# Optimization experiments

Hardware: AMD Instinct MI355X
Metric: run time of the kernel (lower is better)

Reference implementation:

```python
import jax, jax.numpy as jnp
import numpy as np

DEPTH, HEADS, DIM_HEAD = 6, 12, 64
DIM, MLP, FEAT = 768, 3072, 1000
B, N = 32, 196
EPS = 1e-5


def layernorm(x, g, b):
    m = jnp.mean(x, axis=-1, keepdims=True)
    v = jnp.var(x, axis=-1, keepdims=True)
    return (x - m) * jax.lax.rsqrt(v + EPS) * g + b


def setup_inputs() -> dict:
    key = jax.random.key(0)
    ks = jax.random.split(key, 8)
    s = 0.02
    return {
        "x": jax.random.normal(ks[0], (B, N, DIM), jnp.float32),
        "cls_token": jax.random.normal(ks[1], (1, 1, DIM), jnp.float32),
        "ln1_g": jnp.ones((DEPTH, DIM), jnp.float32),
        "ln1_b": jnp.zeros((DEPTH, DIM), jnp.float32),
        "w_qkv": jax.random.normal(ks[2], (DEPTH, DIM, 3 * HEADS * DIM_HEAD), jnp.float32) * s,
        "reattn_w": jax.random.normal(ks[3], (DEPTH, HEADS, HEADS), jnp.float32),
        "reattn_g": jnp.ones((DEPTH, HEADS), jnp.float32),
        "reattn_b": jnp.zeros((DEPTH, HEADS), jnp.float32),
        "w_out": jax.random.normal(ks[4], (DEPTH, HEADS * DIM_HEAD, DIM), jnp.float32) * s,
        "b_out": jnp.zeros((DEPTH, DIM), jnp.float32),
        "ln2_g": jnp.ones((DEPTH, DIM), jnp.float32),
        "ln2_b": jnp.zeros((DEPTH, DIM), jnp.float32),
        "w1": jax.random.normal(ks[5], (DEPTH, DIM, MLP), jnp.float32) * s,
        "b1": jnp.zeros((DEPTH, MLP), jnp.float32),
        "w2": jax.random.normal(ks[6], (DEPTH, MLP, DIM), jnp.float32) * s,
        "b2": jnp.zeros((DEPTH, DIM), jnp.float32),
        "lnf_g": jnp.ones((DIM,), jnp.float32),
        "lnf_b": jnp.zeros((DIM,), jnp.float32),
        "w_head": jax.random.normal(ks[7], (DIM, FEAT), jnp.float32) * s,
        "b_head": jnp.zeros((FEAT,), jnp.float32),
    }


def _forward(x, cls_token, ln1_g, ln1_b, w_qkv, reattn_w, reattn_g, reattn_b,
             w_out, b_out, ln2_g, ln2_b, w1, b1, w2, b2, lnf_g, lnf_b, w_head, b_head):
    b = x.shape[0]
    cls = jnp.broadcast_to(cls_token, (b, 1, DIM))
    x = jnp.concatenate([cls, x], axis=1)  # (B, N+1, DIM)
    n = x.shape[1]
    scale = DIM_HEAD ** -0.5
    for l in range(DEPTH):
        h = layernorm(x, ln1_g[l], ln1_b[l])
        qkv = h @ w_qkv[l]                       # (B, n, 3*H*Dh)
        qkv = qkv.reshape(b, n, 3, HEADS, DIM_HEAD)
        q, k, v = (qkv[:, :, i].transpose(0, 2, 1, 3) for i in range(3))  # b h n d
        dots = jnp.einsum('bhid,bhjd->bhij', q, k) * scale
        attn = jax.nn.softmax(dots, axis=-1)
        attn = jnp.einsum('bhij,hg->bgij', attn, reattn_w[l])
        # per-head LayerNorm: normalize over head axis (axis=1)
        m = jnp.mean(attn, axis=1, keepdims=True)
        var = jnp.var(attn, axis=1, keepdims=True)
        attn = (attn - m) * jax.lax.rsqrt(var + EPS)
        attn = attn * reattn_g[l][None, :, None, None] + reattn_b[l][None, :, None, None]
        out = jnp.einsum('bhij,bhjd->bhid', attn, v)
        out = out.transpose(0, 2, 1, 3).reshape(b, n, HEADS * DIM_HEAD)
        x = x + out @ w_out[l] + b_out[l]
        h = layernorm(x, ln2_g[l], ln2_b[l])
        h = jax.nn.gelu(h @ w1[l] + b1[l], approximate=False)
        x = x + h @ w2[l] + b2[l]
    pooled = x[:, 0]  # cls pool
    return layernorm(pooled, lnf_g, lnf_b) @ w_head + b_head


def reference(x, cls_token, ln1_g, ln1_b, w_qkv, reattn_w, reattn_g, reattn_b,
              w_out, b_out, ln2_g, ln2_b, w1, b1, w2, b2, lnf_g, lnf_b, w_head, b_head):
    return _forward(x, cls_token, ln1_g, ln1_b, w_qkv, reattn_w, reattn_g, reattn_b,
                    w_out, b_out, ln2_g, ln2_b, w1, b1, w2, b2, lnf_g, lnf_b, w_head, b_head)
```

## Files before the change

### kernel.cpp

```cpp
#include <hip/hip_runtime.h>
#include <cstdint>

typedef __bf16 bf16_t;
typedef __bf16 bf16x8 __attribute__((ext_vector_type(8)));
typedef float  f32x4  __attribute__((ext_vector_type(4)));
typedef unsigned int u32;

#define DEPTH 6
#define HEADS 12
#define DH    64
#define DIM   768
#define MLPD  3072
#define FEAT  1000
#define BATCH 32
#define SEQ   197
#define NP    224
#define TOK   (BATCH*SEQ)

__device__ __forceinline__ f32x4 zero4() {
    f32x4 z; z[0] = 0.f; z[1] = 0.f; z[2] = 0.f; z[3] = 0.f; return z;
}

__device__ __forceinline__ f32x4 mfma16(bf16x8 a, bf16x8 b, f32x4 c) {
    return __builtin_amdgcn_mfma_f32_16x16x32_bf16(a, b, c, 0, 0, 0);
}

typedef const __attribute__((address_space(1))) u32* gas_ptr;
typedef __attribute__((address_space(3))) u32*       las_ptr;
__device__ __forceinline__ void gload16(const bf16_t* g, bf16_t* l) {
    __builtin_amdgcn_global_load_lds((gas_ptr)g, (las_ptr)l, 16, 0, 0);
}

__global__ __launch_bounds__(256) void concat_k(const float* __restrict__ x,
                                                const float* __restrict__ cls,
                                                float* __restrict__ xbuf) {
    int idx = blockIdx.x * 256 + threadIdx.x;
    int col = idx % DIM;
    int row = idx / DIM;
    int b = row / SEQ, p = row % SEQ;
    xbuf[idx] = (p == 0) ? cls[col] : x[(b * 196 + p - 1) * DIM + col];
}

__global__ __launch_bounds__(256) void tcvt_k(const float* __restrict__ W,
                                              bf16_t* __restrict__ Wt,
                                              int K, int N) {
    __shared__ float t[32][33];
    int n0 = blockIdx.x * 32, k0 = blockIdx.y * 32;
    int c = threadIdx.x & 31, r = threadIdx.x >> 5;
#pragma unroll
    for (int i = 0; i < 4; i++) {
        int k = k0 + r + i * 8, n = n0 + c;
        t[r + i * 8][c] = (n < N) ? W[k * N + n] : 0.f;
    }
    __syncthreads();
#pragma unroll
    for (int i = 0; i < 4; i++) {
        int n = n0 + r + i * 8, k = k0 + c;
        if (n < N) Wt[n * K + k] = (bf16_t)t[c][r + i * 8];
    }
}

__global__ __launch_bounds__(256) void ln_k(const float* __restrict__ x, long row_stride,
                                            const float* __restrict__ g,
                                            const float* __restrict__ b,
                                            bf16_t* __restrict__ out) {
    int row = blockIdx.x;
    const float* xr = x + (long)row * row_stride;
    int t = threadIdx.x;
    float v0 = xr[t], v1 = xr[t + 256], v2 = xr[t + 512];
    float s  = v0 + v1 + v2;
    float sq = v0 * v0 + v1 * v1 + v2 * v2;
#pragma unroll
    for (int o = 1; o < 64; o <<= 1) { s += __shfl_xor(s, o); sq += __shfl_xor(sq, o); }
    __shared__ float ss[4], sqs[4];
    int w = t >> 6;
    if ((t & 63) == 0) { ss[w] = s; sqs[w] = sq; }
    __syncthreads();
    s  = ss[0] + ss[1] + ss[2] + ss[3];
    sq = sqs[0] + sqs[1] + sqs[2] + sqs[3];
    float m  = s * (1.f / 768.f);
    float rs = rsqrtf(sq * (1.f / 768.f) - m * m + 1e-5f);
    bf16_t* orow = out + (long)row * DIM;
    orow[t]       = (bf16_t)((v0 - m) * rs * g[t]       + b[t]);
    orow[t + 256] = (bf16_t)((v1 - m) * rs * g[t + 256] + b[t + 256]);
    orow[t + 512] = (bf16_t)((v2 - m) * rs * g[t + 512] + b[t + 512]);
}

template <int MODE>
__global__ __launch_bounds__(256) void gemm_k(const bf16_t* __restrict__ A,
                                              const bf16_t* __restrict__ Bt,
                                              const float* __restrict__ bias,
                                              float* __restrict__ Cf,
                                              bf16_t* __restrict__ Cb,
                                              int M, int N, int K) {
    __shared__ bf16_t sA[2][128][32];
    __shared__ bf16_t sB[2][128][32];
    int tid = threadIdx.x;
    int bm = blockIdx.x * 128, bn = blockIdx.y * 128;
    int wave = tid >> 6, lane = tid & 63;
    int wm = (wave >> 1) * 64, wn = (wave & 1) * 64;
    int la = lane & 15, lb = lane >> 4;

    int rowA[2], rowB[2], colE[2];
#pragma unroll
    for (int q = 0; q < 2; q++) {
        int li = (wave * 2 + q) * 64 + lane;
        int row = li >> 2;
        colE[q] = (li & 3) * 8;
        int ar = bm + row; if (ar > M - 1) ar = M - 1;
        int br = bn + row; if (br > N - 1) br = N - 1;
        rowA[q] = ar; rowB[q] = br;
    }

    f32x4 acc[4][4];
#pragma unroll
    for (int m = 0; m < 4; m++)
#pragma unroll
        for (int n = 0; n < 4; n++) acc[m][n] = zero4();

    int nt = K >> 5;

#pragma unroll
    for (int q = 0; q < 2; q++) {
        gload16(A  + (long)rowA[q] * K + colE[q], &sA[0][0][0] + (wave * 2 + q) * 512);
        gload16(Bt + (long)rowB[q] * K + colE[q], &sB[0][0][0] + (wave * 2 + q) * 512);
    }
    __syncthreads();

    for (int t = 0; t < nt; t++) {
        int cur = t & 1;
        if (t + 1 < nt) {
            int k0 = (t + 1) << 5;
#pragma unroll
            for (int q = 0; q < 2; q++) {
                gload16(A  + (long)rowA[q] * K + k0 + colE[q], &sA[cur ^ 1][0][0] + (wave * 2 + q) * 512);
                gload16(Bt + (long)rowB[q] * K + k0 + colE[q], &sB[cur ^ 1][0][0] + (wave * 2 + q) * 512);
            }
        }
        bf16x8 af[4], bfr[4];
#pragma unroll
        for (int m = 0; m < 4; m++) af[m]  = *(const bf16x8*)&sA[cur][wm + m * 16 + la][lb * 8];
#pragma unroll
        for (int n = 0; n < 4; n++) bfr[n] = *(const bf16x8*)&sB[cur][wn + n * 16 + la][lb * 8];
#pragma unroll
        for (int m = 0; m < 4; m++)
#pragma unroll
            for (int n = 0; n < 4; n++)
                acc[m][n] = mfma16(af[m], bfr[n], acc[m][n]);
        __syncthreads();
    }

#pragma unroll
    for (int m = 0; m < 4; m++) {
#pragma unroll
        for (int n = 0; n < 4; n++) {
            int ib = bm + wm + m * 16 + lb * 4;
            int jb = bn + wn + n * 16 + la;
            if (jb >= N) continue;
            float bv = (MODE == 0) ? 0.f : bias[jb];
#pragma unroll
            for (int r = 0; r < 4; r++) {
                int i = ib + r;
                if (i >= M) continue;
                float v = acc[m][n][r];
                if (MODE == 0) {
                    Cb[(long)i * N + jb] = (bf16_t)v;
                } else if (MODE == 1) {
                    Cf[(long)i * N + jb] += v + bv;
                } else if (MODE == 2) {
                    float u = v + bv;
                    Cb[(long)i * N + jb] = (bf16_t)(0.5f * u * (1.f + erff(u * 0.70710678118f)));
                } else {
                    Cf[(long)i * N + jb] = v + bv;
                }
            }
        }
    }
}

__global__ __launch_bounds__(256) void qk_k(const bf16_t* __restrict__ qkv,
                                            float* __restrict__ dots) {
    int bh = blockIdx.z;
    int b = bh / HEADS, h = bh % HEADS;
    int i0 = blockIdx.x * 64, j0 = blockIdx.y * 64;
    __shared__ bf16_t sQ[64][32], sK[64][32];
    int tid = threadIdx.x, wave = tid >> 6, lane = tid & 63;
    int wm = (wave >> 1) * 32, wn = (wave & 1) * 32;
    int la = lane & 15, lb = lane >> 4;
    f32x4 acc[2][2];
#pragma unroll
    for (int m = 0; m < 2; m++)
#pragma unroll
        for (int n = 0; n < 2; n++) acc[m][n] = zero4();

    int row = tid >> 2, col = (tid & 3) * 8;
    int qi = i0 + row; if (qi > SEQ - 1) qi = SEQ - 1;
    int kj = j0 + row; if (kj > SEQ - 1) kj = SEQ - 1;
    const bf16_t* qsrc = qkv + (((b * SEQ + qi) * 3 + 0) * HEADS + h) * DH + col;
    const bf16_t* ksrc = qkv + (((b * SEQ + kj) * 3 + 1) * HEADS + h) * DH + col;

#pragma unroll
    for (int d0 = 0; d0 < 64; d0 += 32) {
        *(bf16x8*)&sQ[row][col] = *(const bf16x8*)(qsrc + d0);
        *(bf16x8*)&sK[row][col] = *(const bf16x8*)(ksrc + d0);
        __syncthreads();
        bf16x8 af[2], bfr[2];
#pragma unroll
        for (int m = 0; m < 2; m++) af[m]  = *(const bf16x8*)&sQ[wm + m * 16 + la][lb * 8];
#pragma unroll
        for (int n = 0; n < 2; n++) bfr[n] = *(const bf16x8*)&sK[wn + n * 16 + la][lb * 8];
#pragma unroll
        for (int m = 0; m < 2; m++)
#pragma unroll
            for (int n = 0; n < 2; n++)
                acc[m][n] = mfma16(af[m], bfr[n], acc[m][n]);
        __syncthreads();
    }
#pragma unroll
    for (int m = 0; m < 2; m++)
#pragma unroll
        for (int n = 0; n < 2; n++)
#pragma unroll
            for (int r = 0; r < 4; r++) {
                int i = i0 + wm + m * 16 + lb * 4 + r;
                int j = j0 + wn + n * 16 + la;
                if (i < SEQ && j < SEQ)
                    dots[((long)bh * SEQ + i) * NP + j] = acc[m][n][r] * 0.125f;
            }
}

__global__ __launch_bounds__(256) void smre_k(const float* __restrict__ dots,
                                              const float* __restrict__ W,
                                              const float* __restrict__ gg,
                                              const float* __restrict__ bb,
                                              bf16_t* __restrict__ attn2) {
    __shared__ float sm[HEADS][NP];
    __shared__ float sW[HEADS * HEADS];
    __shared__ float sg[HEADS], sb[HEADS];
    int tid = threadIdx.x;
    if (tid < HEADS * HEADS) sW[tid] = W[tid];
    if (tid < HEADS) { sg[tid] = gg[tid]; sb[tid] = bb[tid]; }
    int bi = blockIdx.x;
    int b = bi / SEQ, i = bi % SEQ;
    int wave = tid >> 6, lane = tid & 63;

    for (int h = wave; h < HEADS; h += 4) {
        const float* p = dots + ((long)(b * HEADS + h) * SEQ + i) * NP;
        float v[4], e[4];
#pragma unroll
        for (int q = 0; q < 4; q++) { int j = lane + 64 * q; v[q] = (j < SEQ) ? p[j] : -3.0e38f; }
        float mx = fmaxf(fmaxf(v[0], v[1]), fmaxf(v[2], v[3]));
#pragma unroll
        for (int o = 1; o < 64; o <<= 1) mx = fmaxf(mx, __shfl_xor(mx, o));
        float s = 0.f;
#pragma unroll
        for (int q = 0; q < 4; q++) {
            int j = lane + 64 * q;
            e[q] = (j < SEQ) ? __expf(v[q] - mx) : 0.f;
            s += e[q];
        }
#pragma unroll
        for (int o = 1; o < 64; o <<= 1) s += __shfl_xor(s, o);
        float inv = 1.f / s;
#pragma unroll
        for (int q = 0; q < 4; q++) { int j = lane + 64 * q; if (j < NP) sm[h][j] = e[q] * inv; }
    }
    __syncthreads();

    int j = tid;
    if (j >= NP) return;
    bool valid = j < SEQ;
    float vals[HEADS];
#pragma unroll
    for (int h = 0; h < HEADS; h++) vals[h] = valid ? sm[h][j] : 0.f;
    float mix[HEADS];
    float s = 0.f, sq = 0.f;
#pragma unroll
    for (int g = 0; g < HEADS; g++) {
        float a = 0.f;
#pragma unroll
        for (int h = 0; h < HEADS; h++) a += vals[h] * sW[h * HEADS + g];
        mix[g] = a; s += a; sq += a * a;
    }
    float m  = s * (1.f / 12.f);
    float rs = rsqrtf(sq * (1.f / 12.f) - m * m + 1e-5f);
    long base = ((long)(b * HEADS) * SEQ + i) * NP + j;
    const long hs = (long)SEQ * NP;
#pragma unroll
    for (int g = 0; g < HEADS; g++) {
        float o = valid ? ((mix[g] - m) * rs * sg[g] + sb[g]) : 0.f;
        attn2[base + g * hs] = (bf16_t)o;
    }
}

__global__ __launch_bounds__(256) void pv_k(const bf16_t* __restrict__ attn2,
                                            const bf16_t* __restrict__ qkv,
                                            bf16_t* __restrict__ aout) {
    int bh = blockIdx.y;
    int b = bh / HEADS, h = bh % HEADS;
    int i0 = blockIdx.x * 64;
    __shared__ bf16_t sP[64][32];
    __shared__ bf16_t sVt[64][32];
    int tid = threadIdx.x, wave = tid >> 6, lane = tid & 63;
    int wm = (wave >> 1) * 32, wn = (wave & 1) * 32;
    int la = lane & 15, lb = lane >> 4;
    f32x4 acc[2][2];
#pragma unroll
    for (int m = 0; m < 2; m++)
#pragma unroll
        for (int n = 0; n < 2; n++) acc[m][n] = zero4();

    int prow = tid >> 2, pcol = (tid & 3) * 8;
    int pi = i0 + prow; if (pi > SEQ - 1) pi = SEQ - 1;
    const bf16_t* psrc = attn2 + ((long)bh * SEQ + pi) * NP + pcol;
    int jl = tid >> 3, dblk = (tid & 7) * 8;
    int jlx = jl ^ ((tid & 3) << 3);

    for (int j0 = 0; j0 < NP; j0 += 32) {
        *(bf16x8*)&sP[prow][pcol] = *(const bf16x8*)(psrc + j0);
        int jg = j0 + jl;
        bf16x8 vv;
#pragma unroll
        for (int e = 0; e < 8; e++) vv[e] = (bf16_t)0.f;
        if (jg < SEQ)
            vv = *(const bf16x8*)(qkv + (((b * SEQ + jg) * 3 + 2) * HEADS + h) * DH + dblk);
#pragma unroll
        for (int e = 0; e < 8; e++) sVt[dblk + e][jlx] = vv[e];
        __syncthreads();
        bf16x8 af[2], bfr[2];
#pragma unroll
        for (int m = 0; m < 2; m++) af[m] = *(const bf16x8*)&sP[wm + m * 16 + la][lb * 8];
#pragma unroll
        for (int n = 0; n < 2; n++) {
            int rowd = wn + n * 16 + la;
            int colj = (lb * 8) ^ (((rowd >> 3) & 3) << 3);
            bfr[n] = *(const bf16x8*)&sVt[rowd][colj];
        }
#pragma unroll
        for (int m = 0; m < 2; m++)
#pragma unroll
            for (int n = 0; n < 2; n++)
                acc[m][n] = mfma16(af[m], bfr[n], acc[m][n]);
        __syncthreads();
    }
#pragma unroll
    for (int m = 0; m < 2; m++)
#pragma unroll
        for (int n = 0; n < 2; n++)
#pragma unroll
            for (int r = 0; r < 4; r++) {
                int i = i0 + wm + m * 16 + lb * 4 + r;
                int d = wn + n * 16 + la;
                if (i < SEQ)
                    aout[((long)b * SEQ + i) * DIM + h * DH + d] = (bf16_t)acc[m][n][r];
            }
}

extern "C" void kernel_launch(void* const* d_in, const int* in_sizes, int n_in,
                              void* d_out, int out_size, void* d_ws, size_t ws_size,
                              hipStream_t stream) {
    const float* x        = (const float*)d_in[0];
    const float* cls      = (const float*)d_in[1];
    const float* ln1_g    = (const float*)d_in[2];
    const float* ln1_b    = (const float*)d_in[3];
    const float* w_qkv    = (const float*)d_in[4];
    const float* reattn_w = (const float*)d_in[5];
    const float* reattn_g = (const float*)d_in[6];
    const float* reattn_b = (const float*)d_in[7];
    const float* w_out    = (const float*)d_in[8];
    const float* b_out    = (const float*)d_in[9];
    const float* ln2_g    = (const float*)d_in[10];
    const float* ln2_b    = (const float*)d_in[11];
    const float* w1       = (const float*)d_in[12];
    const float* b1       = (const float*)d_in[13];
    const float* w2       = (const float*)d_in[14];
    const float* b2       = (const float*)d_in[15];
    const float* lnf_g    = (const float*)d_in[16];
    const float* lnf_b    = (const float*)d_in[17];
    const float* w_head   = (const float*)d_in[18];
    const float* b_head   = (const float*)d_in[19];
    float* out = (float*)d_out;

    char* p = (char*)d_ws;
    auto alloc = [&](size_t bytes) -> char* {
        char* r = p;
        p += (bytes + 255) & ~(size_t)255;
        return r;
    };
    bf16_t* wt      = (bf16_t*)alloc(2ULL * MLPD * DIM);
    bf16_t* wt_head = (bf16_t*)alloc(2ULL * FEAT * DIM);
    float*  xbuf    = (float*)alloc(4ULL * TOK * DIM);
    bf16_t* h_ln    = (bf16_t*)alloc(2ULL * TOK * DIM);
    bf16_t* qkv     = (bf16_t*)alloc(2ULL * TOK * 3 * DIM);
    float*  dots    = (float*)alloc(4ULL * BATCH * HEADS * SEQ * NP);
    bf16_t* h_mid   = (bf16_t*)dots;
    bf16_t* attn2   = (bf16_t*)alloc(2ULL * BATCH * HEADS * SEQ * NP);
    bf16_t* aout    = (bf16_t*)alloc(2ULL * TOK * DIM);

    dim3 B256(256);
    concat_k<<<(TOK * DIM) / 256, B256, 0, stream>>>(x, cls, xbuf);
    tcvt_k<<<dim3((FEAT + 31) / 32, DIM / 32), B256, 0, stream>>>(w_head, wt_head, DIM, FEAT);

    for (int l = 0; l < DEPTH; l++) {
        ln_k<<<TOK, B256, 0, stream>>>(xbuf, DIM, ln1_g + l * DIM, ln1_b + l * DIM, h_ln);
        tcvt_k<<<dim3(2304 / 32, DIM / 32), B256, 0, stream>>>(w_qkv + (long)l * DIM * 2304, wt, DIM, 2304);
        gemm_k<0><<<dim3(50, 18), B256, 0, stream>>>(h_ln, wt, nullptr, nullptr, qkv, TOK, 2304, DIM);
        qk_k<<<dim3(4, 4, BATCH * HEADS), B256, 0, stream>>>(qkv, dots);
        smre_k<<<TOK, B256, 0, stream>>>(
            dots, reattn_w + l * HEADS * HEADS, reattn_g + l * HEADS, reattn_b + l * HEADS, attn2);
        pv_k<<<dim3(4, BATCH * HEADS), B256, 0, stream>>>(attn2, qkv, aout);
        tcvt_k<<<dim3(DIM / 32, DIM / 32), B256, 0, stream>>>(w_out + (long)l * DIM * DIM, wt, DIM, DIM);
        gemm_k<1><<<dim3(50, 6), B256, 0, stream>>>(aout, wt, b_out + l * DIM, xbuf, nullptr, TOK, DIM, DIM);
        ln_k<<<TOK, B256, 0, stream>>>(xbuf, DIM, ln2_g + l * DIM, ln2_b + l * DIM, h_ln);
        tcvt_k<<<dim3(MLPD / 32, DIM / 32), B256, 0, stream>>>(w1 + (long)l * DIM * MLPD, wt, DIM, MLPD);
        gemm_k<2><<<dim3(50, 24), B256, 0, stream>>>(h_ln, wt, b1 + l * MLPD, nullptr, h_mid, TOK, MLPD, DIM);
        tcvt_k<<<dim3(DIM / 32, MLPD / 32), B256, 0, stream>>>(w2 + (long)l * MLPD * DIM, wt, MLPD, DIM);
        gemm_k<1><<<dim3(50, 6), B256, 0, stream>>>(h_mid, wt, b2 + l * DIM, xbuf, nullptr, TOK, DIM, MLPD);
    }

    ln_k<<<BATCH, B256, 0, stream>>>(xbuf, (long)SEQ * DIM, lnf_g, lnf_b, h_ln);
    gemm_k<3><<<dim3(1, 8), B256, 0, stream>>>(h_ln, wt_head, b_head, out, nullptr, BATCH, FEAT, DIM);
}
```

Measured before the change: 2.143 ms.

## Replace layer GEMMs with 256x256 eight-wave MFMA kernel using swizzled LDS

Adds gemm8_k, a 512-thread kernel that computes 256x256 tiles with BK=64. It uses XOR-swizzled LDS layouts, loads directly from global memory into LDS two stages ahead, and splits each k-step into four MFMA quadrants with barriers and setprio interleaving. The QKV, out-projection, MLP1 and MLP2 GEMMs now use it, while the head GEMM stays on a simplified 128x128 kernel. The goals are more data reuse per tile, fewer LDS bank conflicts and better overlap of loads with MFMA work. The cost is heavy register use at one block per CU and coarse tiles: with 6304 rows there are 25 row tiles, which gives only 75 blocks for the N=768 GEMMs, so the GPU may be underfilled.

```diff
diff --git a/kernel.cpp b/kernel.cpp
--- a/kernel.cpp
+++ b/kernel.cpp
@@ -29,6 +29,11 @@
 typedef __attribute__((address_space(3))) u32*       las_ptr;
 __device__ __forceinline__ void gload16(const bf16_t* g, bf16_t* l) {
     __builtin_amdgcn_global_load_lds((gas_ptr)g, (las_ptr)l, 16, 0, 0);
+}
+
+__device__ __forceinline__ void bar() {
+    __builtin_amdgcn_s_barrier();
+    asm volatile("" ::: "memory");
 }
 
 __global__ __launch_bounds__(256) void concat_k(const float* __restrict__ x,
@@ -86,12 +91,170 @@
     orow[t + 512] = (bf16_t)((v2 - m) * rs * g[t + 512] + b[t + 512]);
 }
 
+#define MFMAQ(mh, nh)                                                        \
+    _Pragma("unroll")                                                        \
+    for (int mf = 0; mf < 4; mf++) {                                         \
+        _Pragma("unroll")                                                    \
+        for (int nf = 0; nf < 2; nf++) {                                     \
+            f32x4 c = acc[(mh) * 2 + (nh)][mf * 2 + nf];                     \
+            c = mfma16(aR[mf][0], bR[nh][nf][0], c);                         \
+            c = mfma16(aR[mf][1], bR[nh][nf][1], c);                         \
+            acc[(mh) * 2 + (nh)][mf * 2 + nf] = c;                           \
+        }                                                                    \
+    }
+
 template <int MODE>
-__global__ __launch_bounds__(256) void gemm_k(const bf16_t* __restrict__ A,
+__global__ __launch_bounds__(512, 1) void gemm8_k(const bf16_t* __restrict__ A,
+                                                  const bf16_t* __restrict__ Bt,
+                                                  const float* __restrict__ bias,
+                                                  float* __restrict__ Cf,
+                                                  bf16_t* __restrict__ Cb,
+                                                  int M, int N, int K, int gn) {
+    __shared__ bf16_t sA[2][256 * 64];
+    __shared__ bf16_t sB[2][256 * 64];
+    int tid = threadIdx.x;
+    int bm = (blockIdx.x / gn) * 256, bn = (blockIdx.x % gn) * 256;
+    int wave = tid >> 6, lane = tid & 63;
+    int wm = (wave >> 2) * 128, wn = (wave & 3) * 64;
+    int la = lane & 15, lb = lane >> 4;
+
+    int srow = tid >> 3;
+    int scol = ((tid & 7) ^ (srow & 7)) * 8;
+    int rA[4], rB[4];
+#pragma unroll
+    for (int i = 0; i < 4; i++) {
+        int r = bm + i * 64 + srow; rA[i] = (r < M) ? r : M - 1;
+        rB[i] = bn + i * 64 + srow;
+    }
+    int woff = wave * 512;
+
+    f32x4 acc[4][8];
+#pragma unroll
+    for (int q = 0; q < 4; q++)
+#pragma unroll
+        for (int f = 0; f < 8; f++) acc[q][f] = zero4();
+    bf16x8 aR[4][2], bR[2][2][2];
+
+    const int NT = K >> 6;
+
+    auto stA = [&](int buf, int kt) {
+        long k0 = (long)kt << 6;
+#pragma unroll
+        for (int i = 0; i < 4; i++)
+            gload16(A + (long)rA[i] * K + k0 + scol, &sA[buf][0] + i * 4096 + woff);
+    };
+    auto stB = [&](int buf, int kt) {
+        long k0 = (long)kt << 6;
+#pragma unroll
+        for (int i = 0; i < 4; i++)
+            gload16(Bt + (long)rB[i] * K + k0 + scol, &sB[buf][0] + i * 4096 + woff);
+    };
+
+    stB(0, 0); stA(0, 0); stB(1, 1); stA(1, 1);
+    asm volatile("s_waitcnt vmcnt(8)" ::: "memory");
+    bar();
+
+    for (int t = 0; t < NT; t++) {
+        const bf16_t* cA = &sA[t & 1][0];
+        const bf16_t* cB = &sB[t & 1][0];
+        bool st = (t + 2) < NT;
+
+#pragma unroll
+        for (int mf = 0; mf < 4; mf++)
+#pragma unroll
+            for (int ks = 0; ks < 2; ks++) {
+                int r = wm + mf * 16 + la, gl = ks * 4 + lb;
+                aR[mf][ks] = *(const bf16x8*)(cA + r * 64 + ((gl ^ (r & 7)) << 3));
+            }
+#pragma unroll
+        for (int nf = 0; nf < 2; nf++)
+#pragma unroll
+            for (int ks = 0; ks < 2; ks++) {
+                int r = wn + nf * 16 + la, gl = ks * 4 + lb;
+                bR[0][nf][ks] = *(const bf16x8*)(cB + r * 64 + ((gl ^ (r & 7)) << 3));
+            }
+        bar();
+        asm volatile("s_waitcnt lgkmcnt(0)" ::: "memory");
+        __builtin_amdgcn_sched_barrier(0);
+        __builtin_amdgcn_s_setprio(1);
+        MFMAQ(0, 0)
+        __builtin_amdgcn_s_setprio(0);
+        bar();
+
+#pragma unroll
+        for (int nf = 0; nf < 2; nf++)
+#pragma unroll
+            for (int ks = 0; ks < 2; ks++) {
+                int r = wn + 32 + nf * 16 + la, gl = ks * 4 + lb;
+                bR[1][nf][ks] = *(const bf16x8*)(cB + r * 64 + ((gl ^ (r & 7)) << 3));
+            }
+        bar();
+        asm volatile("s_waitcnt lgkmcnt(0)" ::: "memory");
+        __builtin_amdgcn_sched_barrier(0);
+        __builtin_amdgcn_s_setprio(1);
+        MFMAQ(0, 1)
+        __builtin_amdgcn_s_setprio(0);
+        bar();
+
+#pragma unroll
+        for (int mf = 0; mf < 4; mf++)
+#pragma unroll
+            for (int ks = 0; ks < 2; ks++) {
+                int r = wm + 64 + mf * 16 + la, gl = ks * 4 + lb;
+                aR[mf][ks] = *(const bf16x8*)(cA + r * 64 + ((gl ^ (r & 7)) << 3));
+            }
+        if (st) stB(t & 1, t + 2);
+        bar();
+        asm volatile("s_waitcnt lgkmcnt(0)" ::: "memory");
+        __builtin_amdgcn_sched_barrier(0);
+        __builtin_amdgcn_s_setprio(1);
+        MFMAQ(1, 1)
+        __builtin_amdgcn_s_setprio(0);
+        bar();
+
+        if (st) stA(t & 1, t + 2);
+        __builtin_amdgcn_s_setprio(1);
+        MFMAQ(1, 0)
+        __builtin_amdgcn_s_setprio(0);
+        if (t < NT - 1) {
+            if (st) asm volatile("s_waitcnt vmcnt(8)" ::: "memory");
+            else    asm volatile("s_waitcnt vmcnt(0)" ::: "memory");
+            bar();
+        }
+    }
+
+#pragma unroll
+    for (int mh = 0; mh < 2; mh++)
+#pragma unroll
+        for (int nh = 0; nh < 2; nh++)
+#pragma unroll
+            for (int mf = 0; mf < 4; mf++)
+#pragma unroll
+                for (int nf = 0; nf < 2; nf++) {
+                    int ib = bm + wm + mh * 64 + mf * 16 + lb * 4;
+                    int jb = bn + wn + nh * 32 + nf * 16 + la;
+                    float bv = (MODE == 0) ? 0.f : bias[jb];
+                    f32x4 v = acc[mh * 2 + nh][mf * 2 + nf];
+#pragma unroll
+                    for (int rr = 0; rr < 4; rr++) {
+                        int i = ib + rr;
+                        if (i >= M) continue;
+                        if (MODE == 0) {
+                            Cb[(long)i * N + jb] = (bf16_t)v[rr];
+                        } else if (MODE == 1) {
+                            Cf[(long)i * N + jb] += v[rr] + bv;
+                        } else {
+                            float u = v[rr] + bv;
+                            Cb[(long)i * N + jb] = (bf16_t)(0.5f * u * (1.f + erff(u * 0.70710678118f)));
+                        }
+                    }
+                }
+}
+
+__global__ __launch_bounds__(256) void gemm_h(const bf16_t* __restrict__ A,
                                               const bf16_t* __restrict__ Bt,
                                               const float* __restrict__ bias,
                                               float* __restrict__ Cf,
-                                              bf16_t* __restrict__ Cb,
                                               int M, int N, int K) {
     __shared__ bf16_t sA[2][128][32];
     __shared__ bf16_t sB[2][128][32];
@@ -100,7 +263,6 @@
     int wave = tid >> 6, lane = tid & 63;
     int wm = (wave >> 1) * 64, wn = (wave & 1) * 64;
     int la = lane & 15, lb = lane >> 4;
-
     int rowA[2], rowB[2], colE[2];
 #pragma unroll
     for (int q = 0; q < 2; q++) {
@@ -111,22 +273,18 @@
         int br = bn + row; if (br > N - 1) br = N - 1;
         rowA[q] = ar; rowB[q] = br;
     }
-
     f32x4 acc[4][4];
 #pragma unroll
     for (int m = 0; m < 4; m++)
 #pragma unroll
         for (int n = 0; n < 4; n++) acc[m][n] = zero4();
-
     int nt = K >> 5;
-
 #pragma unroll
     for (int q = 0; q < 2; q++) {
         gload16(A  + (long)rowA[q] * K + colE[q], &sA[0][0][0] + (wave * 2 + q) * 512);
         gload16(Bt + (long)rowB[q] * K + colE[q], &sB[0][0][0] + (wave * 2 + q) * 512);
     }
     __syncthreads();
-
     for (int t = 0; t < nt; t++) {
         int cur = t & 1;
         if (t + 1 < nt) {
@@ -149,7 +307,6 @@
                 acc[m][n] = mfma16(af[m], bfr[n], acc[m][n]);
         __syncthreads();
     }
-
 #pragma unroll
     for (int m = 0; m < 4; m++) {
 #pragma unroll
@@ -157,22 +314,12 @@
             int ib = bm + wm + m * 16 + lb * 4;
             int jb = bn + wn + n * 16 + la;
             if (jb >= N) continue;
-            float bv = (MODE == 0) ? 0.f : bias[jb];
+            float bv = bias[jb];
 #pragma unroll
             for (int r = 0; r < 4; r++) {
                 int i = ib + r;
                 if (i >= M) continue;
-                float v = acc[m][n][r];
-                if (MODE == 0) {
-                    Cb[(long)i * N + jb] = (bf16_t)v;
-                } else if (MODE == 1) {
-                    Cf[(long)i * N + jb] += v + bv;
-                } else if (MODE == 2) {
-                    float u = v + bv;
-                    Cb[(long)i * N + jb] = (bf16_t)(0.5f * u * (1.f + erff(u * 0.70710678118f)));
-                } else {
-                    Cf[(long)i * N + jb] = v + bv;
-                }
+                Cf[(long)i * N + jb] = acc[m][n][r] + bv;
             }
         }
     }
@@ -397,27 +544,28 @@
     bf16_t* attn2   = (bf16_t*)alloc(2ULL * BATCH * HEADS * SEQ * NP);
     bf16_t* aout    = (bf16_t*)alloc(2ULL * TOK * DIM);
 
-    dim3 B256(256);
+    dim3 B256(256), B512(512);
+    const int GM = (TOK + 255) / 256;
     concat_k<<<(TOK * DIM) / 256, B256, 0, stream>>>(x, cls, xbuf);
     tcvt_k<<<dim3((FEAT + 31) / 32, DIM / 32), B256, 0, stream>>>(w_head, wt_head, DIM, FEAT);
 
     for (int l = 0; l < DEPTH; l++) {
         ln_k<<<TOK, B256, 0, stream>>>(xbuf, DIM, ln1_g + l * DIM, ln1_b + l * DIM, h_ln);
         tcvt_k<<<dim3(2304 / 32, DIM / 32), B256, 0, stream>>>(w_qkv + (long)l * DIM * 2304, wt, DIM, 2304);
-        gemm_k<0><<<dim3(50, 18), B256, 0, stream>>>(h_ln, wt, nullptr, nullptr, qkv, TOK, 2304, DIM);
+        gemm8_k<0><<<GM * 9, B512, 0, stream>>>(h_ln, wt, nullptr, nullptr, qkv, TOK, 2304, DIM, 9);
         qk_k<<<dim3(4, 4, BATCH * HEADS), B256, 0, stream>>>(qkv, dots);
         smre_k<<<TOK, B256, 0, stream>>>(
             dots, reattn_w + l * HEADS * HEADS, reattn_g + l * HEADS, reattn_b + l * HEADS, attn2);
         pv_k<<<dim3(4, BATCH * HEADS), B256, 0, stream>>>(attn2, qkv, aout);
         tcvt_k<<<dim3(DIM / 32, DIM / 32), B256, 0, stream>>>(w_out + (long)l * DIM * DIM, wt, DIM, DIM);
-        gemm_k<1><<<dim3(50, 6), B256, 0, stream>>>(aout, wt, b_out + l * DIM, xbuf, nullptr, TOK, DIM, DIM);
+        gemm8_k<1><<<GM * 3, B512, 0, stream>>>(aout, wt, b_out + l * DIM, xbuf, nullptr, TOK, DIM, DIM, 3);
         ln_k<<<TOK, B256, 0, stream>>>(xbuf, DIM, ln2_g + l * DIM, ln2_b + l * DIM, h_ln);
         tcvt_k<<<dim3(MLPD / 32, DIM / 32), B256, 0, stream>>>(w1 + (long)l * DIM * MLPD, wt, DIM, MLPD);
-        gemm_k<2><<<dim3(50, 24), B256, 0, stream>>>(h_ln, wt, b1 + l * MLPD, nullptr, h_mid, TOK, MLPD, DIM);
+        gemm8_k<2><<<GM * 12, B512, 0, stream>>>(h_ln, wt, b1 + l * MLPD, nullptr, h_mid, TOK, MLPD, DIM, 12);
         tcvt_k<<<dim3(DIM / 32, MLPD / 32), B256, 0, stream>>>(w2 + (long)l * MLPD * DIM, wt, MLPD, DIM);
-        gemm_k<1><<<dim3(50, 6), B256, 0, stream>>>(h_mid, wt, b2 + l * DIM, xbuf, nullptr, TOK, DIM, MLPD);
+        gemm8_k<1><<<GM * 3, B512, 0, stream>>>(h_mid, wt, b2 + l * DIM, xbuf, nullptr, TOK, DIM, MLPD, 3);
     }
 
     ln_k<<<BATCH, B256, 0, stream>>>(xbuf, (long)SEQ * DIM, lnf_g, lnf_b, h_ln);
-    gemm_k<3><<<dim3(1, 8), B256, 0, stream>>>(h_ln, wt_head, b_head, out, nullptr, BATCH, FEAT, DIM);
-}
+    gemm_h<<<dim3(1, 8), B256, 0, stream>>>(h_ln, wt_head, b_head, out, BATCH, FEAT, DIM);
+}
```

New measurement: 2.804 ms. +30.8%, slower.

## Fuse softmax/re-attention with PV matmul and split-K the MLP down projection

Applied to the files above, without the earlier changes.

The separate softmax+re-attention kernel and the PV kernel become one kernel that processes 8 query rows across all 12 heads per block. It keeps the mixed attention probabilities in shared memory and multiplies them with V directly, so the bf16 attn2 intermediate no longer goes through global memory. The MLP second GEMM is split into two K halves across a grid z dimension, writing fp32 partials that a new reduction kernel adds into the residual along with the bias. A dedicated head GEMM kernel replaces the old mode-3 path. The costs are a large shared-memory footprint per block, 8-row MFMA tiles that leave half of each 16-row fragment unused, and extra fp32 partial traffic for the split-K.

```diff
diff --git a/kernel.cpp b/kernel.cpp
--- a/kernel.cpp
+++ b/kernel.cpp
@@ -16,6 +16,7 @@
 #define SEQ   197
 #define NP    224
 #define TOK   (BATCH*SEQ)
+#define ITILES 25
 
 __device__ __forceinline__ f32x4 zero4() {
     f32x4 z; z[0] = 0.f; z[1] = 0.f; z[2] = 0.f; z[3] = 0.f; return z;
@@ -92,11 +93,12 @@
                                               const float* __restrict__ bias,
                                               float* __restrict__ Cf,
                                               bf16_t* __restrict__ Cb,
-                                              int M, int N, int K) {
+                                              int M, int N, int Kstride, int Klen) {
     __shared__ bf16_t sA[2][128][32];
     __shared__ bf16_t sB[2][128][32];
     int tid = threadIdx.x;
     int bm = blockIdx.x * 128, bn = blockIdx.y * 128;
+    long koff = (long)blockIdx.z * Klen;
     int wave = tid >> 6, lane = tid & 63;
     int wm = (wave >> 1) * 64, wn = (wave & 1) * 64;
     int la = lane & 15, lb = lane >> 4;
@@ -118,23 +120,21 @@
 #pragma unroll
         for (int n = 0; n < 4; n++) acc[m][n] = zero4();
 
-    int nt = K >> 5;
-
+    int nt = Klen >> 5;
 #pragma unroll
     for (int q = 0; q < 2; q++) {
-        gload16(A  + (long)rowA[q] * K + colE[q], &sA[0][0][0] + (wave * 2 + q) * 512);
-        gload16(Bt + (long)rowB[q] * K + colE[q], &sB[0][0][0] + (wave * 2 + q) * 512);
+        gload16(A  + (long)rowA[q] * Kstride + koff + colE[q], &sA[0][0][0] + (wave * 2 + q) * 512);
+        gload16(Bt + (long)rowB[q] * Kstride + koff + colE[q], &sB[0][0][0] + (wave * 2 + q) * 512);
     }
     __syncthreads();
-
     for (int t = 0; t < nt; t++) {
         int cur = t & 1;
         if (t + 1 < nt) {
-            int k0 = (t + 1) << 5;
+            long k0 = koff + ((t + 1) << 5);
 #pragma unroll
             for (int q = 0; q < 2; q++) {
-                gload16(A  + (long)rowA[q] * K + k0 + colE[q], &sA[cur ^ 1][0][0] + (wave * 2 + q) * 512);
-                gload16(Bt + (long)rowB[q] * K + k0 + colE[q], &sB[cur ^ 1][0][0] + (wave * 2 + q) * 512);
+                gload16(A  + (long)rowA[q] * Kstride + k0 + colE[q], &sA[cur ^ 1][0][0] + (wave * 2 + q) * 512);
+                gload16(Bt + (long)rowB[q] * Kstride + k0 + colE[q], &sB[cur ^ 1][0][0] + (wave * 2 + q) * 512);
             }
         }
         bf16x8 af[4], bfr[4];
@@ -150,6 +150,7 @@
         __syncthreads();
     }
 
+    long kout = (long)blockIdx.z * M * (long)N;
 #pragma unroll
     for (int m = 0; m < 4; m++) {
 #pragma unroll
@@ -157,7 +158,7 @@
             int ib = bm + wm + m * 16 + lb * 4;
             int jb = bn + wn + n * 16 + la;
             if (jb >= N) continue;
-            float bv = (MODE == 0) ? 0.f : bias[jb];
+            float bv = (MODE == 1 || MODE == 2) ? bias[jb] : 0.f;
 #pragma unroll
             for (int r = 0; r < 4; r++) {
                 int i = ib + r;
@@ -171,8 +172,92 @@
                     float u = v + bv;
                     Cb[(long)i * N + jb] = (bf16_t)(0.5f * u * (1.f + erff(u * 0.70710678118f)));
                 } else {
-                    Cf[(long)i * N + jb] = v + bv;
+                    Cf[kout + (long)i * N + jb] = v;
                 }
+            }
+        }
+    }
+}
+
+__global__ __launch_bounds__(256) void redk_k(float* __restrict__ xbuf,
+                                              const float* __restrict__ part,
+                                              const float* __restrict__ bias) {
+    const long total = (long)TOK * DIM;
+    for (long idx = blockIdx.x * 256 + threadIdx.x; idx < total; idx += (long)gridDim.x * 256) {
+        int col = (int)(idx % DIM);
+        xbuf[idx] += part[idx] + part[idx + total] + bias[col];
+    }
+}
+
+__global__ __launch_bounds__(256) void gemm_h(const bf16_t* __restrict__ A,
+                                              const bf16_t* __restrict__ Bt,
+                                              const float* __restrict__ bias,
+                                              float* __restrict__ Cf,
+                                              int M, int N, int K) {
+    __shared__ bf16_t sA[2][128][32];
+    __shared__ bf16_t sB[2][128][32];
+    int tid = threadIdx.x;
+    int bm = blockIdx.x * 128, bn = blockIdx.y * 128;
+    int wave = tid >> 6, lane = tid & 63;
+    int wm = (wave >> 1) * 64, wn = (wave & 1) * 64;
+    int la = lane & 15, lb = lane >> 4;
+    int rowA[2], rowB[2], colE[2];
+#pragma unroll
+    for (int q = 0; q < 2; q++) {
+        int li = (wave * 2 + q) * 64 + lane;
+        int row = li >> 2;
+        colE[q] = (li & 3) * 8;
+        int ar = bm + row; if (ar > M - 1) ar = M - 1;
+        int br = bn + row; if (br > N - 1) br = N - 1;
+        rowA[q] = ar; rowB[q] = br;
+    }
+    f32x4 acc[4][4];
+#pragma unroll
+    for (int m = 0; m < 4; m++)
+#pragma unroll
+        for (int n = 0; n < 4; n++) acc[m][n] = zero4();
+    int nt = K >> 5;
+#pragma unroll
+    for (int q = 0; q < 2; q++) {
+        gload16(A  + (long)rowA[q] * K + colE[q], &sA[0][0][0] + (wave * 2 + q) * 512);
+        gload16(Bt + (long)rowB[q] * K + colE[q], &sB[0][0][0] + (wave * 2 + q) * 512);
+    }
+    __syncthreads();
+    for (int t = 0; t < nt; t++) {
+        int cur = t & 1;
+        if (t + 1 < nt) {
+            int k0 = (t + 1) << 5;
+#pragma unroll
+            for (int q = 0; q < 2; q++) {
+                gload16(A  + (long)rowA[q] * K + k0 + colE[q], &sA[cur ^ 1][0][0] + (wave * 2 + q) * 512);
+                gload16(Bt + (long)rowB[q] * K + k0 + colE[q], &sB[cur ^ 1][0][0] + (wave * 2 + q) * 512);
+            }
+        }
+        bf16x8 af[4], bfr[4];
+#pragma unroll
+        for (int m = 0; m < 4; m++) af[m]  = *(const bf16x8*)&sA[cur][wm + m * 16 + la][lb * 8];
+#pragma unroll
+        for (int n = 0; n < 4; n++) bfr[n] = *(const bf16x8*)&sB[cur][wn + n * 16 + la][lb * 8];
+#pragma unroll
+        for (int m = 0; m < 4; m++)
+#pragma unroll
+            for (int n = 0; n < 4; n++)
+                acc[m][n] = mfma16(af[m], bfr[n], acc[m][n]);
+        __syncthreads();
+    }
+#pragma unroll
+    for (int m = 0; m < 4; m++) {
+#pragma unroll
+        for (int n = 0; n < 4; n++) {
+            int ib = bm + wm + m * 16 + lb * 4;
+            int jb = bn + wn + n * 16 + la;
+            if (jb >= N) continue;
+            float bv = bias[jb];
+#pragma unroll
+            for (int r = 0; r < 4; r++) {
+                int i = ib + r;
+                if (i >= M) continue;
+                Cf[(long)i * N + jb] = acc[m][n][r] + bv;
             }
         }
     }
@@ -229,131 +314,135 @@
             }
 }
 
-__global__ __launch_bounds__(256) void smre_k(const float* __restrict__ dots,
-                                              const float* __restrict__ W,
-                                              const float* __restrict__ gg,
-                                              const float* __restrict__ bb,
-                                              bf16_t* __restrict__ attn2) {
-    __shared__ float sm[HEADS][NP];
+__global__ __launch_bounds__(256) void smrepv_k(const float* __restrict__ dots,
+                                                const bf16_t* __restrict__ qkv,
+                                                const float* __restrict__ W,
+                                                const float* __restrict__ gg,
+                                                const float* __restrict__ bb,
+                                                bf16_t* __restrict__ aout) {
+    __shared__ __align__(16) float  sm[HEADS][8][NP];
+    __shared__ __align__(16) bf16_t sP[HEADS][8][NP];
+    __shared__ __align__(16) bf16_t sVt[4][64][32];
     __shared__ float sW[HEADS * HEADS];
     __shared__ float sg[HEADS], sb[HEADS];
     int tid = threadIdx.x;
     if (tid < HEADS * HEADS) sW[tid] = W[tid];
     if (tid < HEADS) { sg[tid] = gg[tid]; sb[tid] = bb[tid]; }
-    int bi = blockIdx.x;
-    int b = bi / SEQ, i = bi % SEQ;
+    int b = blockIdx.x / ITILES, it = blockIdx.x % ITILES;
+    int i0 = it * 8;
     int wave = tid >> 6, lane = tid & 63;
+    int nrow = SEQ - i0; if (nrow > 8) nrow = 8;
 
     for (int h = wave; h < HEADS; h += 4) {
-        const float* p = dots + ((long)(b * HEADS + h) * SEQ + i) * NP;
-        float v[4], e[4];
-#pragma unroll
-        for (int q = 0; q < 4; q++) { int j = lane + 64 * q; v[q] = (j < SEQ) ? p[j] : -3.0e38f; }
-        float mx = fmaxf(fmaxf(v[0], v[1]), fmaxf(v[2], v[3]));
-#pragma unroll
-        for (int o = 1; o < 64; o <<= 1) mx = fmaxf(mx, __shfl_xor(mx, o));
-        float s = 0.f;
-#pragma unroll
-        for (int q = 0; q < 4; q++) {
-            int j = lane + 64 * q;
-            e[q] = (j < SEQ) ? __expf(v[q] - mx) : 0.f;
-            s += e[q];
-        }
-#pragma unroll
-        for (int o = 1; o < 64; o <<= 1) s += __shfl_xor(s, o);
-        float inv = 1.f / s;
-#pragma unroll
-        for (int q = 0; q < 4; q++) { int j = lane + 64 * q; if (j < NP) sm[h][j] = e[q] * inv; }
+        for (int r = 0; r < 8; r++) {
+            if (r >= nrow) {
+#pragma unroll
+                for (int q = 0; q < 4; q++) { int j = lane + 64 * q; if (j < NP) sm[h][r][j] = 0.f; }
+                continue;
+            }
+            const float* p = dots + ((long)(b * HEADS + h) * SEQ + i0 + r) * NP;
+            float v[4], e[4];
+#pragma unroll
+            for (int q = 0; q < 4; q++) { int j = lane + 64 * q; v[q] = (j < SEQ) ? p[j] : -3.0e38f; }
+            float mx = fmaxf(fmaxf(v[0], v[1]), fmaxf(v[2], v[3]));
+#pragma unroll
+            for (int o = 1; o < 64; o <<= 1) mx = fmaxf(mx, __shfl_xor(mx, o));
+            float s = 0.f;
+#pragma unroll
+            for (int q = 0; q < 4; q++) {
+                int j = lane + 64 * q;
+                e[q] = (j < SEQ) ? __expf(v[q] - mx) : 0.f;
+                s += e[q];
+            }
+#pragma unroll
+            for (int o = 1; o < 64; o <<= 1) s += __shfl_xor(s, o);
+            float inv = 1.f / s;
+#pragma unroll
+            for (int q = 0; q < 4; q++) { int j = lane + 64 * q; if (j < NP) sm[h][r][j] = e[q] * inv; }
+        }
     }
     __syncthreads();
 
-    int j = tid;
-    if (j >= NP) return;
-    bool valid = j < SEQ;
-    float vals[HEADS];
-#pragma unroll
-    for (int h = 0; h < HEADS; h++) vals[h] = valid ? sm[h][j] : 0.f;
-    float mix[HEADS];
-    float s = 0.f, sq = 0.f;
-#pragma unroll
-    for (int g = 0; g < HEADS; g++) {
-        float a = 0.f;
-#pragma unroll
-        for (int h = 0; h < HEADS; h++) a += vals[h] * sW[h * HEADS + g];
-        mix[g] = a; s += a; sq += a * a;
-    }
-    float m  = s * (1.f / 12.f);
-    float rs = rsqrtf(sq * (1.f / 12.f) - m * m + 1e-5f);
-    long base = ((long)(b * HEADS) * SEQ + i) * NP + j;
-    const long hs = (long)SEQ * NP;
-#pragma unroll
-    for (int g = 0; g < HEADS; g++) {
-        float o = valid ? ((mix[g] - m) * rs * sg[g] + sb[g]) : 0.f;
-        attn2[base + g * hs] = (bf16_t)o;
-    }
-}
-
-__global__ __launch_bounds__(256) void pv_k(const bf16_t* __restrict__ attn2,
-                                            const bf16_t* __restrict__ qkv,
-                                            bf16_t* __restrict__ aout) {
-    int bh = blockIdx.y;
-    int b = bh / HEADS, h = bh % HEADS;
-    int i0 = blockIdx.x * 64;
-    __shared__ bf16_t sP[64][32];
-    __shared__ bf16_t sVt[64][32];
-    int tid = threadIdx.x, wave = tid >> 6, lane = tid & 63;
-    int wm = (wave >> 1) * 32, wn = (wave & 1) * 32;
+    if (tid < NP) {
+        int j = tid;
+        bool valid = j < SEQ;
+        for (int r = 0; r < 8; r++) {
+            float vals[HEADS];
+#pragma unroll
+            for (int h = 0; h < HEADS; h++) vals[h] = valid ? sm[h][r][j] : 0.f;
+            float mix[HEADS];
+            float s = 0.f, sq = 0.f;
+#pragma unroll
+            for (int g = 0; g < HEADS; g++) {
+                float a = 0.f;
+#pragma unroll
+                for (int h = 0; h < HEADS; h++) a += vals[h] * sW[h * HEADS + g];
+                mix[g] = a; s += a; sq += a * a;
+            }
+            float m  = s * (1.f / 12.f);
+            float rs = rsqrtf(sq * (1.f / 12.f) - m * m + 1e-5f);
+#pragma unroll
+            for (int g = 0; g < HEADS; g++)
+                sP[g][r][j] = (bf16_t)(valid ? ((mix[g] - m) * rs * sg[g] + sb[g]) : 0.f);
+        }
+    }
+    __syncthreads();
+
     int la = lane & 15, lb = lane >> 4;
-    f32x4 acc[2][2];
-#pragma unroll
-    for (int m = 0; m < 2; m++)
-#pragma unroll
-        for (int n = 0; n < 2; n++) acc[m][n] = zero4();
-
-    int prow = tid >> 2, pcol = (tid & 3) * 8;
-    int pi = i0 + prow; if (pi > SEQ - 1) pi = SEQ - 1;
-    const bf16_t* psrc = attn2 + ((long)bh * SEQ + pi) * NP + pcol;
-    int jl = tid >> 3, dblk = (tid & 7) * 8;
-    int jlx = jl ^ ((tid & 3) << 3);
-
-    for (int j0 = 0; j0 < NP; j0 += 32) {
-        *(bf16x8*)&sP[prow][pcol] = *(const bf16x8*)(psrc + j0);
-        int jg = j0 + jl;
-        bf16x8 vv;
-#pragma unroll
-        for (int e = 0; e < 8; e++) vv[e] = (bf16_t)0.f;
-        if (jg < SEQ)
-            vv = *(const bf16x8*)(qkv + (((b * SEQ + jg) * 3 + 2) * HEADS + h) * DH + dblk);
-#pragma unroll
-        for (int e = 0; e < 8; e++) sVt[dblk + e][jlx] = vv[e];
-        __syncthreads();
-        bf16x8 af[2], bfr[2];
-#pragma unroll
-        for (int m = 0; m < 2; m++) af[m] = *(const bf16x8*)&sP[wm + m * 16 + la][lb * 8];
-#pragma unroll
-        for (int n = 0; n < 2; n++) {
-            int rowd = wn + n * 16 + la;
-            int colj = (lb * 8) ^ (((rowd >> 3) & 3) << 3);
-            bfr[n] = *(const bf16x8*)&sVt[rowd][colj];
-        }
-#pragma unroll
-        for (int m = 0; m < 2; m++)
-#pragma unroll
-            for (int n = 0; n < 2; n++)
-                acc[m][n] = mfma16(af[m], bfr[n], acc[m][n]);
-        __syncthreads();
-    }
-#pragma unroll
-    for (int m = 0; m < 2; m++)
-#pragma unroll
-        for (int n = 0; n < 2; n++)
-#pragma unroll
-            for (int r = 0; r < 4; r++) {
-                int i = i0 + wm + m * 16 + lb * 4 + r;
-                int d = wn + n * 16 + la;
-                if (i < SEQ)
-                    aout[((long)b * SEQ + i) * DIM + h * DH + d] = (bf16_t)acc[m][n][r];
-            }
+    f32x4 acc[3][4];
+#pragma unroll
+    for (int hi = 0; hi < 3; hi++)
+#pragma unroll
+        for (int nf = 0; nf < 4; nf++) acc[hi][nf] = zero4();
+
+    for (int hi = 0; hi < 3; hi++) {
+        int g = wave + hi * 4;
+        for (int j0 = 0; j0 < NP; j0 += 32) {
+#pragma unroll
+            for (int c = 0; c < 4; c++) {
+                int idx = c * 64 + lane;
+                int jloc = idx >> 3;
+                int dchunk = idx & 7;
+                int jg = j0 + jloc;
+                bf16x8 vv;
+#pragma unroll
+                for (int e2 = 0; e2 < 8; e2++) vv[e2] = (bf16_t)0.f;
+                if (jg < SEQ)
+                    vv = *(const bf16x8*)(qkv + (((long)(b * SEQ + jg) * 3 + 2) * HEADS + g) * DH + dchunk * 8);
+                int jlx = jloc ^ ((dchunk & 3) << 3);
+#pragma unroll
+                for (int e2 = 0; e2 < 8; e2++) sVt[wave][dchunk * 8 + e2][jlx] = vv[e2];
+            }
+            bf16x8 af;
+            if (la < 8) af = *(const bf16x8*)&sP[g][la][j0 + lb * 8];
+            else {
+#pragma unroll
+                for (int e2 = 0; e2 < 8; e2++) af[e2] = (bf16_t)0.f;
+            }
+#pragma unroll
+            for (int nf = 0; nf < 4; nf++) {
+                int rowd = nf * 16 + la;
+                int colj = (lb * 8) ^ (((rowd >> 3) & 3) << 3);
+                bf16x8 bfr = *(const bf16x8*)&sVt[wave][rowd][colj];
+                acc[hi][nf] = mfma16(af, bfr, acc[hi][nf]);
+            }
+        }
+    }
+#pragma unroll
+    for (int hi = 0; hi < 3; hi++) {
+        int g = wave + hi * 4;
+#pragma unroll
+        for (int nf = 0; nf < 4; nf++) {
+#pragma unroll
+            for (int rr = 0; rr < 4; rr++) {
+                int row = lb * 4 + rr;
+                if (row < nrow) {
+                    int d = nf * 16 + la;
+                    aout[((long)b * SEQ + i0 + row) * DIM + g * DH + d] = (bf16_t)acc[hi][nf][rr];
+                }
+            }
+        }
+    }
 }
 
 extern "C" void kernel_launch(void* const* d_in, const int* in_sizes, int n_in,
@@ -394,7 +483,7 @@
     bf16_t* qkv     = (bf16_t*)alloc(2ULL * TOK * 3 * DIM);
     float*  dots    = (float*)alloc(4ULL * BATCH * HEADS * SEQ * NP);
     bf16_t* h_mid   = (bf16_t*)dots;
-    bf16_t* attn2   = (bf16_t*)alloc(2ULL * BATCH * HEADS * SEQ * NP);
+    float*  part    = (float*)alloc(8ULL * TOK * DIM);
     bf16_t* aout    = (bf16_t*)alloc(2ULL * TOK * DIM);
 
     dim3 B256(256);
@@ -404,20 +493,21 @@
     for (int l = 0; l < DEPTH; l++) {
         ln_k<<<TOK, B256, 0, stream>>>(xbuf, DIM, ln1_g + l * DIM, ln1_b + l * DIM, h_ln);
         tcvt_k<<<dim3(2304 / 32, DIM / 32), B256, 0, stream>>>(w_qkv + (long)l * DIM * 2304, wt, DIM, 2304);
-        gemm_k<0><<<dim3(50, 18), B256, 0, stream>>>(h_ln, wt, nullptr, nullptr, qkv, TOK, 2304, DIM);
+        gemm_k<0><<<dim3(50, 18), B256, 0, stream>>>(h_ln, wt, nullptr, nullptr, qkv, TOK, 2304, DIM, DIM);
         qk_k<<<dim3(4, 4, BATCH * HEADS), B256, 0, stream>>>(qkv, dots);
-        smre_k<<<TOK, B256, 0, stream>>>(
-            dots, reattn_w + l * HEADS * HEADS, reattn_g + l * HEADS, reattn_b + l * HEADS, attn2);
-        pv_k<<<dim3(4, BATCH * HEADS), B256, 0, stream>>>(attn2, qkv, aout);
+        smrepv_k<<<BATCH * ITILES, B256, 0, stream>>>(
+            dots, qkv, reattn_w + l * HEADS * HEADS, reattn_g + l * HEADS, reattn_b + l * HEADS, aout);
         tcvt_k<<<dim3(DIM / 32, DIM / 32), B256, 0, stream>>>(w_out + (long)l * DIM * DIM, wt, DIM, DIM);
-        gemm_k<1><<<dim3(50, 6), B256, 0, stream>>>(aout, wt, b_out + l * DIM, xbuf, nullptr, TOK, DIM, DIM);
+        gemm_k<1><<<dim3(50, 6), B256, 0, stream>>>(aout, wt, b_out + l * DIM, xbuf, nullptr, TOK, DIM, DIM, DIM);
         ln_k<<<TOK, B256, 0, stream>>>(xbuf, DIM, ln2_g + l * DIM, ln2_b + l * DIM, h_ln);
         tcvt_k<<<dim3(MLPD / 32, DIM / 32), B256, 0, stream>>>(w1 + (long)l * DIM * MLPD, wt, DIM, MLPD);
-        gemm_k<2><<<dim3(50, 24), B256, 0, stream>>>(h_ln, wt, b1 + l * MLPD, nullptr, h_mid, TOK, MLPD, DIM);
+        gemm_k<2><<<dim3(50, 24), B256, 0, stream>>>(h_ln, wt, b1 + l * MLPD, nullptr, h_mid, TOK, MLPD, DIM, DIM);
         tcvt_k<<<dim3(DIM / 32, MLPD / 32), B256, 0, stream>>>(w2 + (long)l * MLPD * DIM, wt, MLPD, DIM);
-        gemm_k<1><<<dim3(50, 6), B256, 0, stream>>>(h_mid, wt, b2 + l * DIM, xbuf, nullptr, TOK, DIM, MLPD);
+        gemm_k<3><<<dim3(50, 6, 2), B256, 0, stream>>>(h_mid, wt, nullptr, part, nullptr,
+                                                       TOK, DIM, MLPD, MLPD / 2);
+        redk_k<<<2048, B256, 0, stream>>>(xbuf, part, b2 + l * DIM);
     }
 
     ln_k<<<BATCH, B256, 0, stream>>>(xbuf, (long)SEQ * DIM, lnf_g, lnf_b, h_ln);
-    gemm_k<3><<<dim3(1, 8), B256, 0, stream>>>(h_ln, wt_head, b_head, out, nullptr, BATCH, FEAT, DIM);
-}
+    gemm_h<<<dim3(1, 8), B256, 0, stream>>>(h_ln, wt_head, b_head, out, BATCH, FEAT, DIM);
+}
```

After: 2.796 ms. 1.3x slower.
